# Kernel optimization log

Measured on AMD Instinct MI355X. Metric: run time of the kernel, lower is better.

The kernel has to match this reference:

```python
import jax, jax.numpy as jnp
import numpy as np

B, S, D = 4, 4096, 256


def setup_inputs() -> dict:
    key = jax.random.key(0)
    k1, k2, k3, k4, k5 = jax.random.split(key, 5)
    query = jax.random.normal(k1, (B, S, D), dtype=jnp.float32)
    key_t = jax.random.normal(k2, (B, S, D), dtype=jnp.float32)
    value = jax.random.normal(k3, (B, S, D), dtype=jnp.float32)
    # nn.Linear(dim_model, dim_model): weight [D, D] (out, in), bias [D]
    bound = 1.0 / np.sqrt(D)
    Wq = jax.random.uniform(k4, (D, D), dtype=jnp.float32, minval=-bound, maxval=bound)
    bq = jax.random.uniform(k5, (D,), dtype=jnp.float32, minval=-bound, maxval=bound)
    return {"query": query, "key": key_t, "value": value, "Wq": Wq, "bq": bq}


def reference(query, key, value, Wq, bq):
    # Faithful to source: self.q is applied to ALL THREE inputs (source bug).
    q = jnp.einsum('bsd,od->bso', query, Wq) + bq  # [B,S,D]
    k = jnp.einsum('bsd,od->bso', key, Wq) + bq
    v = jnp.einsum('bsd,od->bso', value, Wq) + bq
    scale = jnp.sqrt(jnp.asarray(q.shape[-1], q.dtype))
    scores = jnp.einsum('bqd,bkd->bqk', q, k) / scale  # [B,S,S]
    attn = jax.nn.softmax(scores, axis=-1)
    return jnp.einsum('bqk,bkd->bqd', attn, v)  # [B,S,D]
```

## Files before the change

### kernel.cpp

```cpp
#include <hip/hip_runtime.h>


typedef __attribute__((ext_vector_type(4)))  float    f32x4;
typedef __attribute__((ext_vector_type(16))) float    f32x16;
typedef __attribute__((ext_vector_type(8)))  short    s16x8;
typedef __attribute__((ext_vector_type(2)))  unsigned u32x2;

#define AS_GLB const __attribute__((address_space(1))) unsigned
#define AS_LDS __attribute__((address_space(3))) unsigned

static constexpr float CEXP = 0.09016844f;
static constexpr float CM   = -32.0f * 0.09016844f;

static constexpr size_t QBF_OFF = 0;
static constexpr size_t KBF_OFF = 8ull  << 20;
static constexpr size_t VTB_OFF = 16ull << 20;
static constexpr size_t OT_OFF  = 24ull << 20;
static constexpr size_t LS_OFF  = 56ull << 20;

__device__ __forceinline__ unsigned bf16_rne(float f) {
  union { float f; unsigned u; } v; v.f = f;
  return (v.u + 0x7FFFu + ((v.u >> 16) & 1u)) >> 16;
}
__device__ __forceinline__ unsigned pkbf16(float a, float b) {
  return bf16_rne(a) | (bf16_rne(b) << 16);
}

__global__ __launch_bounds__(256, 2) void proj_kernel(
    const float* __restrict__ Xq, const float* __restrict__ Xk,
    const float* __restrict__ Xv, const float* __restrict__ Wq,
    const float* __restrict__ bq, char* __restrict__ ws)
{
  __shared__ char plds[32768];
  const int tid = threadIdx.x;
  const int lane = tid & 63, w = tid >> 6;
  const int wr = w >> 1, wc = w & 1;
  const int l15 = lane & 15, l4 = (lane >> 4) & 3;

  const int mt = blockIdx.x;
  const int tensor = mt >> 7;
  const int r0 = (mt & 127) << 7;
  const int n0 = blockIdx.y << 7;
  const float* A = (tensor == 0) ? Xq : (tensor == 1 ? Xk : Xv);

  f32x4 acc[4][4];
#pragma unroll
  for (int i = 0; i < 4; ++i)
#pragma unroll
    for (int j = 0; j < 4; ++j) { acc[i][j][0]=0.f; acc[i][j][1]=0.f; acc[i][j][2]=0.f; acc[i][j][3]=0.f; }

  for (int kt = 0; kt < 4; ++kt) {
    const int k0 = kt << 6;
#pragma unroll
    for (int j = 0; j < 8; ++j) {
      int c = j * 256 + tid;
      int row = c >> 4, col4 = c & 15;
      f32x4 av = *(const f32x4*)(A + (size_t)(r0 + row) * 256 + k0 + col4 * 4);
      u32x2 pa; pa[0] = pkbf16(av[0], av[1]); pa[1] = pkbf16(av[2], av[3]);
      int off = row * 128 + ((col4 * 8) ^ ((row & 7) << 4));
      *(u32x2*)(plds + off) = pa;
      f32x4 wv = *(const f32x4*)(Wq + (size_t)(n0 + row) * 256 + k0 + col4 * 4);
      u32x2 pw; pw[0] = pkbf16(wv[0], wv[1]); pw[1] = pkbf16(wv[2], wv[3]);
      *(u32x2*)(plds + 16384 + off) = pw;
    }
    __syncthreads();
#pragma unroll
    for (int ks = 0; ks < 2; ++ks) {
      s16x8 af[4], wf[4];
#pragma unroll
      for (int mi = 0; mi < 4; ++mi) {
        int row = wr * 64 + mi * 16 + l15;
        af[mi] = *(const s16x8*)(plds + row * 128 + ((ks * 64 + l4 * 16) ^ ((row & 7) << 4)));
      }
#pragma unroll
      for (int ni = 0; ni < 4; ++ni) {
        int row = wc * 64 + ni * 16 + l15;
        wf[ni] = *(const s16x8*)(plds + 16384 + row * 128 + ((ks * 64 + l4 * 16) ^ ((row & 7) << 4)));
      }
      if (tensor == 1) {
#pragma unroll
        for (int mi = 0; mi < 4; ++mi)
#pragma unroll
          for (int ni = 0; ni < 4; ++ni)
            acc[mi][ni] = __builtin_amdgcn_mfma_f32_16x16x32_bf16(wf[ni], af[mi], acc[mi][ni], 0, 0, 0);
      } else {
#pragma unroll
        for (int mi = 0; mi < 4; ++mi)
#pragma unroll
          for (int ni = 0; ni < 4; ++ni)
            acc[mi][ni] = __builtin_amdgcn_mfma_f32_16x16x32_bf16(af[mi], wf[ni], acc[mi][ni], 0, 0, 0);
      }
    }
    __syncthreads();
  }

  if (tensor == 0) {
    unsigned short* Qb = (unsigned short*)(ws + QBF_OFF);
#pragma unroll
    for (int ni = 0; ni < 4; ++ni) {
      int gn = n0 + wc * 64 + ni * 16 + l15;
      float bias = bq[gn];
#pragma unroll
      for (int mi = 0; mi < 4; ++mi) {
        int mrow = r0 + wr * 64 + mi * 16 + l4 * 4;
#pragma unroll
        for (int j = 0; j < 4; ++j)
          Qb[(size_t)(mrow + j) * 256 + gn] = (unsigned short)bf16_rne(acc[mi][ni][j] + bias);
      }
    }
  } else if (tensor == 1) {
    char* Kf = ws + KBF_OFF;
#pragma unroll
    for (int ni = 0; ni < 4; ++ni) {
      int dbase = n0 + wc * 64 + ni * 16 + l4 * 4;
      f32x4 bv = *(const f32x4*)(bq + dbase);
#pragma unroll
      for (int mi = 0; mi < 4; ++mi) {
        int s = r0 + wr * 64 + mi * 16 + l15;
        int b2 = s >> 12, sl = s & 31, kb = (s & 4095) >> 5;
        size_t chunk = (((size_t)b2 * 128 + kb) * 32 + (dbase >> 3)) * 32 + sl;
        u32x2 pv;
        pv[0] = pkbf16(acc[mi][ni][0] + bv[0], acc[mi][ni][1] + bv[1]);
        pv[1] = pkbf16(acc[mi][ni][2] + bv[2], acc[mi][ni][3] + bv[3]);
        *(u32x2*)(Kf + chunk * 16 + (dbase & 7) * 2) = pv;
      }
    }
  } else {
    char* Vf = ws + VTB_OFF;
#pragma unroll
    for (int ni = 0; ni < 4; ++ni) {
      int gn = n0 + wc * 64 + ni * 16 + l15;
      float bias = bq[gn];
#pragma unroll
      for (int mi = 0; mi < 4; ++mi) {
        int s = r0 + wr * 64 + mi * 16 + l4 * 4;
        int b2 = s >> 12, kb = (s & 4095) >> 5, sl = s & 31;
        size_t chunk = ((((size_t)b2 * 128 + kb) * 4 + (sl >> 3)) * 8 + (gn >> 5)) * 32 + (gn & 31);
        u32x2 pv;
        pv[0] = pkbf16(acc[mi][ni][0] + bias, acc[mi][ni][1] + bias);
        pv[1] = pkbf16(acc[mi][ni][2] + bias, acc[mi][ni][3] + bias);
        *(u32x2*)(Vf + chunk * 16 + (sl & 7) * 2) = pv;
      }
    }
  }
}

__global__ __launch_bounds__(256, 2) void flash_kernel(char* __restrict__ ws)
{
  __shared__ char lds[65536];
  const int tid = threadIdx.x;
  const int lane = tid & 63, w = tid >> 6;
  const int l31 = lane & 31, h = lane >> 5;

  const int bid  = blockIdx.x;
  const int sp   = bid & 3;
  const int b    = (bid >> 2) & 3;
  const int qblk = bid >> 4;
  const int q0w  = qblk * 128 + w * 32;
  const int kb0  = sp * 32;

  const char* Kfb = ws + KBF_OFF + (size_t)b * (2u << 20);
  const char* Vfb = ws + VTB_OFF + (size_t)b * (2u << 20);

  s16x8 qf[16];
  {
    const char* qrow = ws + QBF_OFF + (size_t)((b << 12) + q0w + l31) * 512 + h * 16;
#pragma unroll
    for (int i = 0; i < 16; ++i) qf[i] = *(const s16x8*)(qrow + i * 32);
  }

  f32x16 O[8];
#pragma unroll
  for (int t8 = 0; t8 < 8; ++t8)
#pragma unroll
    for (int r = 0; r < 16; ++r) O[t8][r] = 0.f;

  float l_run = 0.f;

  auto STAGE = [&](int buf, int t) {
    const char* ksrc = Kfb + (size_t)(kb0 + t) * 16384;
    const char* vsrc = Vfb + (size_t)(kb0 + t) * 16384;
#pragma unroll
    for (int i = 0; i < 4; ++i) {
      unsigned c = (unsigned)(w * 4 + i) << 10;
      __builtin_amdgcn_global_load_lds((AS_GLB*)(ksrc + c + (unsigned)lane * 16),
          (AS_LDS*)(lds + buf * 32768 + c), 16, 0, 0);
      __builtin_amdgcn_global_load_lds((AS_GLB*)(vsrc + c + (unsigned)lane * 16),
          (AS_LDS*)(lds + buf * 32768 + 16384 + c), 16, 0, 0);
    }
  };

  auto COMPUTE = [&](int buf) {
    const char* kb = lds + buf * 32768;
    const char* vb = kb + 16384;
    f32x16 pe, po;
#pragma unroll
    for (int r = 0; r < 16; ++r) { pe[r] = 0.f; po[r] = 0.f; }
    __builtin_amdgcn_s_setprio(1);
#pragma unroll
    for (int i = 0; i < 16; i += 2) {
      s16x8 kf0 = *(const s16x8*)(kb + (2 * i + h) * 512 + l31 * 16);
      pe = __builtin_amdgcn_mfma_f32_32x32x16_bf16(kf0, qf[i], pe, 0, 0, 0);
      s16x8 kf1 = *(const s16x8*)(kb + (2 * (i + 1) + h) * 512 + l31 * 16);
      po = __builtin_amdgcn_mfma_f32_32x32x16_bf16(kf1, qf[i + 1], po, 0, 0, 0);
    }
    __builtin_amdgcn_s_setprio(0);
    float p[16]; float sig = 0.f;
#pragma unroll
    for (int r = 0; r < 16; ++r) {
      float e = __builtin_exp2f(__builtin_fmaf(pe[r] + po[r], CEXP, CM));
      p[r] = e; sig += e;
    }
    sig += __shfl_xor(sig, 32, 64);
    l_run += sig;
    unsigned a0, a1, b0, b1, c0, c1, d0, d1;
    asm("v_cvt_pk_bf16_f32 %0, %1, %2" : "=v"(a0) : "v"(p[0]),  "v"(p[1]));
    asm("v_cvt_pk_bf16_f32 %0, %1, %2" : "=v"(a1) : "v"(p[2]),  "v"(p[3]));
    asm("v_cvt_pk_bf16_f32 %0, %1, %2" : "=v"(b0) : "v"(p[4]),  "v"(p[5]));
    asm("v_cvt_pk_bf16_f32 %0, %1, %2" : "=v"(b1) : "v"(p[6]),  "v"(p[7]));
    asm("v_cvt_pk_bf16_f32 %0, %1, %2" : "=v"(c0) : "v"(p[8]),  "v"(p[9]));
    asm("v_cvt_pk_bf16_f32 %0, %1, %2" : "=v"(c1) : "v"(p[10]), "v"(p[11]));
    asm("v_cvt_pk_bf16_f32 %0, %1, %2" : "=v"(d0) : "v"(p[12]), "v"(p[13]));
    asm("v_cvt_pk_bf16_f32 %0, %1, %2" : "=v"(d1) : "v"(p[14]), "v"(p[15]));
    asm("v_permlane32_swap_b32 %0, %1" : "+v"(a0), "+v"(b0));
    asm("v_permlane32_swap_b32 %0, %1" : "+v"(a1), "+v"(b1));
    asm("v_permlane32_swap_b32 %0, %1" : "+v"(c0), "+v"(d0));
    asm("v_permlane32_swap_b32 %0, %1" : "+v"(c1), "+v"(d1));
    union { s16x8 v; unsigned u[4]; } pa0, pa1;
    pa0.u[0] = a0; pa0.u[1] = a1; pa0.u[2] = b0; pa0.u[3] = b1;
    pa1.u[0] = c0; pa1.u[1] = c1; pa1.u[2] = d0; pa1.u[3] = d1;
    __builtin_amdgcn_s_setprio(1);
#pragma unroll
    for (int t8 = 0; t8 < 8; ++t8) {
      s16x8 v0 = *(const s16x8*)(vb + ((h * 8 + t8) << 9) + l31 * 16);
      O[t8] = __builtin_amdgcn_mfma_f32_32x32x16_bf16(pa0.v, v0, O[t8], 0, 0, 0);
      s16x8 v1 = *(const s16x8*)(vb + (((2 + h) * 8 + t8) << 9) + l31 * 16);
      O[t8] = __builtin_amdgcn_mfma_f32_32x32x16_bf16(pa1.v, v1, O[t8], 0, 0, 0);
    }
    __builtin_amdgcn_s_setprio(0);
  };

  STAGE(0, 0);
  __syncthreads();
  for (int t = 0; t < 32; ++t) {
    if (t + 1 < 32) STAGE((t + 1) & 1, t + 1);
    COMPUTE(t & 1);
    __syncthreads();
  }

  unsigned short* OTb = (unsigned short*)(ws + OT_OFF) +
                        (((size_t)(sp * 4 + b) << 12) << 8);
#pragma unroll
  for (int t8 = 0; t8 < 8; ++t8) {
    int d = t8 * 32 + l31;
#pragma unroll
    for (int r = 0; r < 16; ++r) {
      int q = q0w + (r & 3) + 8 * (r >> 2) + 4 * h;
      OTb[(size_t)q * 256 + d] = (unsigned short)bf16_rne(O[t8][r]);
    }
  }
  if (lane < 32) {
    int idx = ((sp * 4 + b) << 12) + q0w + l31;
    ((float*)(ws + LS_OFF))[idx] = l_run;
  }
}

__global__ __launch_bounds__(256) void merge_kernel(const char* __restrict__ ws,
                                                    float* __restrict__ out)
{
  const int t = threadIdx.x;
  const int b = blockIdx.x;
  const int s0 = blockIdx.y << 4;
  const int soff = t >> 7, dd = (t & 127) * 2;
  const unsigned short* OTb = (const unsigned short*)(ws + OT_OFF);
  const float* Ls = (const float*)(ws + LS_OFF);
  for (int si = 0; si < 8; ++si) {
    int s = s0 + si * 2 + soff;
    float L = 0.f;
#pragma unroll
    for (int sp = 0; sp < 4; ++sp) L += Ls[((sp * 4 + b) << 12) + s];
    float rL = 1.0f / L;
    float a0 = 0.f, a1 = 0.f;
#pragma unroll
    for (int sp = 0; sp < 4; ++sp) {
      unsigned uv = *(const unsigned*)(OTb + ((((size_t)(sp * 4 + b) << 12) + s) << 8) + dd);
      union { unsigned u; float f; } lo, hi;
      lo.u = uv << 16; hi.u = uv & 0xFFFF0000u;
      a0 += lo.f; a1 += hi.f;
    }
    float2 o; o.x = a0 * rL; o.y = a1 * rL;
    *(float2*)(out + (((size_t)(b << 12) + s) << 8) + dd) = o;
  }
}

extern "C" void kernel_launch(void* const* d_in, const int* in_sizes, int n_in,
                              void* d_out, int out_size, void* d_ws, size_t ws_size,
                              hipStream_t stream) {
  const float* q  = (const float*)d_in[0];
  const float* k  = (const float*)d_in[1];
  const float* v  = (const float*)d_in[2];
  const float* Wq = (const float*)d_in[3];
  const float* bq = (const float*)d_in[4];
  char* ws = (char*)d_ws;
  float* out = (float*)d_out;
  hipLaunchKernelGGL(proj_kernel, dim3(384, 2), dim3(256), 0, stream, q, k, v, Wq, bq, ws);
  hipLaunchKernelGGL(flash_kernel, dim3(512), dim3(256), 0, stream, ws);
  hipLaunchKernelGGL(merge_kernel, dim3(4, 256), dim3(256), 0, stream, ws, out);
}
```

Baseline: 114.9 us.

## Overlap next-tile global-to-LDS loads with compute using partial vmcnt waits

Replaces the full __syncthreads after each staging with s_waitcnt vmcnt(8) plus raw s_barrier, so the prefetch for the next K/V tile stays in flight while the current tile is computed. The last iteration is peeled to wait on everything. The per-tile row-sum shuffle is moved out of the loop into one cross-half shuffle at the end, and the sum uses a tree of adds. An empty asm pins the Q fragments in registers. It relies on the exact number of outstanding loads per STAGE (8), which is fragile if the load count changes.

```diff
diff --git a/kernel.cpp b/kernel.cpp
--- a/kernel.cpp
+++ b/kernel.cpp
@@ -168,6 +168,8 @@
 #pragma unroll
     for (int i = 0; i < 16; ++i) qf[i] = *(const s16x8*)(qrow + i * 32);
   }
+#pragma unroll
+  for (int i = 0; i < 16; ++i) asm volatile("" :: "v"(qf[i]));
 
   f32x16 O[8];
 #pragma unroll
@@ -205,14 +207,15 @@
       po = __builtin_amdgcn_mfma_f32_32x32x16_bf16(kf1, qf[i + 1], po, 0, 0, 0);
     }
     __builtin_amdgcn_s_setprio(0);
-    float p[16]; float sig = 0.f;
-#pragma unroll
-    for (int r = 0; r < 16; ++r) {
-      float e = __builtin_exp2f(__builtin_fmaf(pe[r] + po[r], CEXP, CM));
-      p[r] = e; sig += e;
-    }
-    sig += __shfl_xor(sig, 32, 64);
-    l_run += sig;
+    float p[16];
+#pragma unroll
+    for (int r = 0; r < 16; ++r)
+      p[r] = __builtin_exp2f(__builtin_fmaf(pe[r] + po[r], CEXP, CM));
+    float s0 = (p[0] + p[1]) + (p[2] + p[3]);
+    float s1 = (p[4] + p[5]) + (p[6] + p[7]);
+    float s2 = (p[8] + p[9]) + (p[10] + p[11]);
+    float s3 = (p[12] + p[13]) + (p[14] + p[15]);
+    l_run += (s0 + s1) + (s2 + s3);
     unsigned a0, a1, b0, b1, c0, c1, d0, d1;
     asm("v_cvt_pk_bf16_f32 %0, %1, %2" : "=v"(a0) : "v"(p[0]),  "v"(p[1]));
     asm("v_cvt_pk_bf16_f32 %0, %1, %2" : "=v"(a1) : "v"(p[2]),  "v"(p[3]));
@@ -241,12 +244,21 @@
   };
 
   STAGE(0, 0);
-  __syncthreads();
-  for (int t = 0; t < 32; ++t) {
-    if (t + 1 < 32) STAGE((t + 1) & 1, t + 1);
+  for (int t = 0; t < 31; ++t) {
+    STAGE((t + 1) & 1, t + 1);
+    asm volatile("s_waitcnt vmcnt(8)" ::: "memory");
+    __builtin_amdgcn_s_barrier();
+    __builtin_amdgcn_sched_barrier(0);
     COMPUTE(t & 1);
-    __syncthreads();
-  }
+    __builtin_amdgcn_s_barrier();
+    __builtin_amdgcn_sched_barrier(0);
+  }
+  asm volatile("s_waitcnt vmcnt(0)" ::: "memory");
+  __builtin_amdgcn_s_barrier();
+  __builtin_amdgcn_sched_barrier(0);
+  COMPUTE(1);
+
+  l_run += __shfl_xor(l_run, 32, 64);
 
   unsigned short* OTb = (unsigned short*)(ws + OT_OFF) +
                         (((size_t)(sp * 4 + b) << 12) << 8);
```

Measured after the change: 112.3 us, median of 2. -2.3%, faster.
